# Kernel optimization log

Measured on AMD Instinct MI355X. Metric: run time of the kernel, lower is better.

Reference implementation:

```python
import jax, jax.numpy as jnp
import numpy as np

B, N, D_IN, D_OUT, H = 64, 512, 256, 256, 4
HD = D_OUT // H


def setup_inputs() -> dict:
    key = jax.random.key(0)
    ks = jax.random.split(key, 10)
    x = jax.random.normal(ks[0], (B, N, D_IN), dtype=jnp.float32)
    adj = jax.random.randint(ks[1], (N, N), 0, 2, dtype=jnp.int32)
    adj = adj.at[jnp.arange(N), jnp.arange(N)].set(1)  # self-loops: no empty rows
    s_in = 1.0 / np.sqrt(D_IN)
    s_out = 1.0 / np.sqrt(D_OUT)
    wq = jax.random.uniform(ks[2], (D_OUT, D_IN), jnp.float32, -s_in, s_in)
    bq = jax.random.uniform(ks[3], (D_OUT,), jnp.float32, -s_in, s_in)
    wk = jax.random.uniform(ks[4], (D_OUT, D_IN), jnp.float32, -s_in, s_in)
    bk = jax.random.uniform(ks[5], (D_OUT,), jnp.float32, -s_in, s_in)
    wv = jax.random.uniform(ks[6], (D_OUT, D_IN), jnp.float32, -s_in, s_in)
    bv = jax.random.uniform(ks[7], (D_OUT,), jnp.float32, -s_in, s_in)
    wo = jax.random.uniform(ks[8], (D_OUT, D_OUT), jnp.float32, -s_out, s_out)
    bo = jax.random.uniform(ks[9], (D_OUT,), jnp.float32, -s_out, s_out)
    return {"x": x, "adj": adj, "wq": wq, "bq": bq, "wk": wk, "bk": bk,
            "wv": wv, "bv": bv, "wo": wo, "bo": bo}


def reference(x, adj, wq, bq, wk, bk, wv, bv, wo, bo):
    b, n, _ = x.shape
    # [B,N,D_out] -> [B,H,N,HD]
    q = (x @ wq.T + bq).reshape(b, n, H, HD).transpose(0, 2, 1, 3)
    k = (x @ wk.T + bk).reshape(b, n, H, HD).transpose(0, 2, 1, 3)
    v = (x @ wv.T + bv).reshape(b, n, H, HD).transpose(0, 2, 1, 3)
    scores = jnp.einsum('bhnd,bhmd->bhnm', q, k) / jnp.sqrt(jnp.float32(HD))
    scores = jnp.where(adj[None, None] == 0, -jnp.inf, scores)
    attn = jnp.nan_to_num(jax.nn.softmax(scores, axis=-1), nan=0.0)
    out = jnp.einsum('bhnm,bhmd->bhnd', attn, v)
    out = out.transpose(0, 2, 1, 3).reshape(b, n, D_OUT)
    return out @ wo.T + bo
```

## Files before the change

kernel.cpp:

```cpp
#include <hip/hip_runtime.h>
#include <stdint.h>

typedef float f32x4 __attribute__((ext_vector_type(4)));
typedef short s16x8 __attribute__((ext_vector_type(8)));
typedef unsigned short u16x4 __attribute__((ext_vector_type(4)));
typedef unsigned int u32x4 __attribute__((ext_vector_type(4)));

#define BB 64
#define NN 512
#define DIN 256
#define DOUT 256
#define HH 4
#define HD 64

__device__ __forceinline__ unsigned short f2b(float f) {
  union { float f; unsigned u; } v; v.f = f;
  unsigned r = v.u + 0x7fffu + ((v.u >> 16) & 1u);
  return (unsigned short)(r >> 16);
}
__device__ __forceinline__ void mfma16(f32x4& acc, s16x8 a, s16x8 b) {
  acc = __builtin_amdgcn_mfma_f32_16x16x32_bf16(a, b, acc, 0, 0, 0);
}
__device__ __forceinline__ unsigned cvtpk(float lo, float hi) {
  unsigned r;
  asm("v_cvt_pk_bf16_f32 %0, %1, %2" : "=v"(r) : "v"(lo), "v"(hi));
  return r;
}

__global__ void k_wconv(const float* __restrict__ s0, const float* __restrict__ s1,
                        const float* __restrict__ s2, const float* __restrict__ s3,
                        unsigned short* __restrict__ d0, unsigned short* __restrict__ d1,
                        unsigned short* __restrict__ d2, unsigned short* __restrict__ d3) {
  int b = blockIdx.x;
  int mat = b >> 6;
  int i = (b & 63) * 256 + threadIdx.x;
  const float* s = mat == 0 ? s0 : mat == 1 ? s1 : mat == 2 ? s2 : s3;
  unsigned short* d = mat == 0 ? d0 : mat == 1 ? d1 : mat == 2 ? d2 : d3;
  f32x4 v = ((const f32x4*)s)[i];
  u16x4 o;
  o[0] = f2b(v[0]); o[1] = f2b(v[1]); o[2] = f2b(v[2]); o[3] = f2b(v[3]);
  ((u16x4*)d)[i] = o;
}

__global__ void k_adjbits(const int* __restrict__ adj, unsigned long long* __restrict__ ab) {
  int row = blockIdx.x;
  int w = threadIdx.x >> 6, lane = threadIdx.x & 63;
  int v = adj[row * NN + w * 64 + lane];
  unsigned long long m = __ballot(v != 0);
  if (lane == 0) ab[row * 8 + w] = m;
}

__global__ __launch_bounds__(256, 2) void k_qkv(
    const float* __restrict__ x,
    const unsigned short* __restrict__ wqh,
    const unsigned short* __restrict__ wkh,
    const unsigned short* __restrict__ wvh,
    const float* __restrict__ bq, const float* __restrict__ bk, const float* __restrict__ bv,
    unsigned short* __restrict__ Qb, unsigned short* __restrict__ Kb, unsigned short* __restrict__ Vtb)
{
  __shared__ __align__(16) unsigned char xs[32768];
  __shared__ __align__(16) unsigned char wsl[32768];
  int tid = threadIdx.x, wave = tid >> 6, lane = tid & 63;
  int lr = lane & 15, lk = lane >> 4;
  int t0 = blockIdx.x * 64;

  const float* xsrc = x + (size_t)t0 * DIN;
#pragma unroll
  for (int i = 0; i < 8; ++i) {
    int lin = i * 256 + tid;
    int r = lin >> 5, cc = lin & 31;
    int dst = r * 512 + ((cc ^ (r & 7)) << 4);
    f32x4 a = *(const f32x4*)(xsrc + lin * 8);
    f32x4 b = *(const f32x4*)(xsrc + lin * 8 + 4);
    u32x4 pk;
    pk[0] = cvtpk(a[0], a[1]); pk[1] = cvtpk(a[2], a[3]);
    pk[2] = cvtpk(b[0], b[1]); pk[3] = cvtpk(b[2], b[3]);
    *(u32x4*)(xs + dst) = pk;
    *(s16x8*)(wsl + dst) = *(const s16x8*)(wqh + lin * 8);
  }
  __syncthreads();

  for (int c = 0; c < 12; ++c) {
    int seg = c >> 2, h = c & 3, nb0 = h * 64;
    const float* bias = seg == 0 ? bq : (seg == 1 ? bk : bv);

    s16x8 gw[8];
    if (c < 11) {
      int cn = c + 1, segn = cn >> 2;
      const unsigned short* wn = (segn == 0 ? wqh : segn == 1 ? wkh : wvh) + (size_t)(cn & 3) * 64 * DIN;
#pragma unroll
      for (int i = 0; i < 8; ++i) gw[i] = *(const s16x8*)(wn + (i * 256 + tid) * 8);
    }

    f32x4 acc[4] = {};
    if (seg < 2) {
      int chrow = wave * 16 + lr;
#pragma unroll
      for (int k0 = 0; k0 < 8; ++k0) {
        int cg = k0 * 4 + lk;
        s16x8 a = *(const s16x8*)(wsl + chrow * 512 + ((cg ^ (chrow & 7)) << 4));
#pragma unroll
        for (int ct = 0; ct < 4; ++ct) {
          int tr = ct * 16 + lr;
          s16x8 b = *(const s16x8*)(xs + tr * 512 + ((cg ^ (tr & 7)) << 4));
          mfma16(acc[ct], a, b);
        }
      }
      unsigned short* dst = (seg == 0) ? Qb : Kb;
      f32x4 bv4 = *(const f32x4*)(bias + nb0 + wave * 16 + lk * 4);
#pragma unroll
      for (int ct = 0; ct < 4; ++ct) {
        int n_ = t0 + ct * 16 + lr;
        int b_ = n_ >> 9, nn = n_ & 511;
        u16x4 pk;
#pragma unroll
        for (int j = 0; j < 4; ++j) pk[j] = f2b(acc[ct][j] + bv4[j]);
        *(u16x4*)(dst + ((size_t)(b_ * HH + h) * NN + nn) * HD + wave * 16 + lk * 4) = pk;
      }
    } else {
      int tokrow = wave * 16 + lr;
#pragma unroll
      for (int k0 = 0; k0 < 8; ++k0) {
        int cg = k0 * 4 + lk;
        s16x8 a = *(const s16x8*)(xs + tokrow * 512 + ((cg ^ (tokrow & 7)) << 4));
#pragma unroll
        for (int nt = 0; nt < 4; ++nt) {
          int cr = nt * 16 + lr;
          s16x8 b = *(const s16x8*)(wsl + cr * 512 + ((cg ^ (cr & 7)) << 4));
          mfma16(acc[nt], a, b);
        }
      }
      int m0 = t0 + wave * 16 + lk * 4;
      int b_ = m0 >> 9, n0 = m0 & 511;
#pragma unroll
      for (int nt = 0; nt < 4; ++nt) {
        int hd = nt * 16 + lr;
        float bs = bias[nb0 + hd];
        u16x4 pk;
#pragma unroll
        for (int j = 0; j < 4; ++j) pk[j] = f2b(acc[nt][j] + bs);
        *(u16x4*)(Vtb + ((size_t)(b_ * HH + h) * HD + hd) * NN + n0) = pk;
      }
    }
    __syncthreads();
    if (c < 11) {
#pragma unroll
      for (int i = 0; i < 8; ++i) {
        int lin = i * 256 + tid;
        int r = lin >> 5, cc = lin & 31;
        *(s16x8*)(wsl + r * 512 + ((cc ^ (r & 7)) << 4)) = gw[i];
      }
    }
    __syncthreads();
  }
}

__global__ __launch_bounds__(512, 2) void k_attn(
    const unsigned short* __restrict__ Qb, const unsigned short* __restrict__ Kb,
    const unsigned short* __restrict__ Vtb, const unsigned long long* __restrict__ ab,
    unsigned short* __restrict__ att)
{
  __shared__ __align__(16) unsigned char kl[2][8192];
  __shared__ __align__(16) unsigned char vtl[2][8192];
  __shared__ __align__(16) unsigned char plb[32768];

  int tid = threadIdx.x, wave = tid >> 6, lane = tid & 63;
  int lr = lane & 15, lk = lane >> 4;
  int bid = blockIdx.x;
  int g = bid >> 4, r = bid & 15;
  int bh = g * 8 + (r & 7);
  int qt = r >> 3;
  int h = bh & 3, b_ = bh >> 2;
  const unsigned short* Qp = Qb + (size_t)bh * NN * HD;
  const unsigned short* Kp = Kb + (size_t)bh * NN * HD;
  const unsigned short* Vp = Vtb + (size_t)bh * HD * NN;
  int q0 = qt * 256 + wave * 32;

  s16x8 qa[2][2];
#pragma unroll
  for (int s = 0; s < 2; ++s) {
    qa[s][0] = *(const s16x8*)(Qp + (q0 + s * 16 + lr) * HD + lk * 8);
    qa[s][1] = *(const s16x8*)(Qp + (q0 + s * 16 + lr) * HD + 32 + lk * 8);
  }

  f32x4 oacc[2][4] = {};
  float rs[2] = {0.f, 0.f};
  unsigned char* plw = plb + wave * 4096;
  int sw = (lr & 7) << 4;

  int srow = tid >> 3, scol = tid & 7;
  int sdst = srow * 128 + ((scol * 16) ^ ((srow & 7) << 4));
  const unsigned short* ksrc = Kp + srow * HD + scol * 8;
  const unsigned short* vsrc = Vp + srow * NN + scol * 8;

  *(s16x8*)(kl[0] + sdst)  = *(const s16x8*)ksrc;
  *(s16x8*)(vtl[0] + sdst) = *(const s16x8*)vsrc;
  __syncthreads();

#pragma unroll
  for (int kt = 0; kt < 8; ++kt) {
    unsigned char* klc = kl[kt & 1];
    unsigned char* vtc = vtl[kt & 1];
    unsigned long long abr[2];
#pragma unroll
    for (int s = 0; s < 2; ++s) abr[s] = ab[(size_t)(q0 + s * 16 + lr) * 8 + kt];

#pragma unroll
    for (int s = 0; s < 2; ++s) {
#pragma unroll
      for (int ks = 0; ks < 4; ++ks) {
        int key = ks * 16 + lr;
        s16x8 kb0 = *(const s16x8*)(klc + key * 128 + ((lk * 16) ^ ((key & 7) << 4)));
        s16x8 kb1 = *(const s16x8*)(klc + key * 128 + ((64 + lk * 16) ^ ((key & 7) << 4)));
        f32x4 sx = {};
        mfma16(sx, kb0, qa[s][0]);
        mfma16(sx, kb1, qa[s][1]);
        float p[4];
#pragma unroll
        for (int j = 0; j < 4; ++j)
          p[j] = ((abr[s] >> (ks * 16 + lk * 4 + j)) & 1ULL) ? __expf(sx[j] * 0.125f) : 0.0f;
        unsigned w0 = cvtpk(p[0], p[1]);
        unsigned w1 = cvtpk(p[2], p[3]);
        union { unsigned u; float f; } t0, t1, t2, t3;
        t0.u = w0 << 16; t1.u = w0 & 0xffff0000u;
        t2.u = w1 << 16; t3.u = w1 & 0xffff0000u;
        rs[s] += (t0.f + t1.f) + (t2.f + t3.f);
        uint2 pw; pw.x = w0; pw.y = w1;
        *(uint2*)(plw + s * 2048 + lr * 128 + ((ks * 32 + lk * 8) ^ sw)) = pw;
      }
    }

    s16x8 gk, gv;
    if (kt < 7) {
      gk = *(const s16x8*)(ksrc + (kt + 1) * 64 * HD);
      gv = *(const s16x8*)(vsrc + (kt + 1) * 64);
    }

#pragma unroll
    for (int s = 0; s < 2; ++s) {
      s16x8 pa0 = *(const s16x8*)(plw + s * 2048 + lr * 128 + ((lk * 16) ^ sw));
      s16x8 pa1 = *(const s16x8*)(plw + s * 2048 + lr * 128 + ((64 + lk * 16) ^ sw));
#pragma unroll
      for (int dt = 0; dt < 4; ++dt) {
        int d = dt * 16 + lr;
        s16x8 vb0 = *(const s16x8*)(vtc + d * 128 + ((lk * 16) ^ ((d & 7) << 4)));
        s16x8 vb1 = *(const s16x8*)(vtc + d * 128 + ((64 + lk * 16) ^ ((d & 7) << 4)));
        mfma16(oacc[s][dt], vb0, pa0);
        mfma16(oacc[s][dt], vb1, pa1);
      }
    }
    if (kt < 7) {
      *(s16x8*)(kl[(kt & 1) ^ 1] + sdst)  = gk;
      *(s16x8*)(vtl[(kt & 1) ^ 1] + sdst) = gv;
      __syncthreads();
    }
  }

#pragma unroll
  for (int s = 0; s < 2; ++s) {
    float v = rs[s];
    v += __shfl_xor(v, 16);
    v += __shfl_xor(v, 32);
    float rinv = 1.0f / v;
    int n_ = q0 + s * 16 + lr;
#pragma unroll
    for (int dt = 0; dt < 4; ++dt) {
      uint2 ow;
      ow.x = cvtpk(oacc[s][dt][0] * rinv, oacc[s][dt][1] * rinv);
      ow.y = cvtpk(oacc[s][dt][2] * rinv, oacc[s][dt][3] * rinv);
      *(uint2*)(att + ((size_t)(b_ * NN + n_) * DOUT) + h * HD + dt * 16 + lk * 4) = ow;
    }
  }
}

__global__ __launch_bounds__(256, 2) void k_out(
    const unsigned short* __restrict__ att, const unsigned short* __restrict__ woh,
    const float* __restrict__ bo, float* __restrict__ out)
{
  __shared__ __align__(16) unsigned char as_[32768];
  __shared__ __align__(16) unsigned char wsl[32768];
  int tid = threadIdx.x, wave = tid >> 6, lane = tid & 63;
  int lr = lane & 15, lk = lane >> 4;
  int t0 = blockIdx.x * 64;

  const unsigned short* asrc = att + (size_t)t0 * DOUT;
#pragma unroll
  for (int i = 0; i < 8; ++i) {
    int lin = i * 256 + tid;
    int r = lin >> 5, cc = lin & 31;
    int dst = r * 512 + ((cc ^ (r & 7)) << 4);
    *(s16x8*)(as_ + dst) = *(const s16x8*)(asrc + lin * 8);
    *(s16x8*)(wsl + dst) = *(const s16x8*)(woh + lin * 8);
  }
  __syncthreads();

  for (int c = 0; c < 4; ++c) {
    int nb0 = c * 64;
    s16x8 gw[8];
    if (c < 3) {
      const unsigned short* wn = woh + (size_t)(c + 1) * 64 * DOUT;
#pragma unroll
      for (int i = 0; i < 8; ++i) gw[i] = *(const s16x8*)(wn + (i * 256 + tid) * 8);
    }

    f32x4 acc[4] = {};
    int chrow = wave * 16 + lr;
#pragma unroll
    for (int k0 = 0; k0 < 8; ++k0) {
      int cg = k0 * 4 + lk;
      s16x8 a = *(const s16x8*)(wsl + chrow * 512 + ((cg ^ (chrow & 7)) << 4));
#pragma unroll
      for (int ct = 0; ct < 4; ++ct) {
        int tr = ct * 16 + lr;
        s16x8 b = *(const s16x8*)(as_ + tr * 512 + ((cg ^ (tr & 7)) << 4));
        mfma16(acc[ct], a, b);
      }
    }
    f32x4 bv4 = *(const f32x4*)(bo + nb0 + wave * 16 + lk * 4);
#pragma unroll
    for (int ct = 0; ct < 4; ++ct) {
      int m = t0 + ct * 16 + lr;
      f32x4 o = acc[ct] + bv4;
      *(f32x4*)(out + (size_t)m * DOUT + nb0 + wave * 16 + lk * 4) = o;
    }
    __syncthreads();
    if (c < 3) {
#pragma unroll
      for (int i = 0; i < 8; ++i) {
        int lin = i * 256 + tid;
        int r = lin >> 5, cc = lin & 31;
        *(s16x8*)(wsl + r * 512 + ((cc ^ (r & 7)) << 4)) = gw[i];
      }
    }
    __syncthreads();
  }
}

extern "C" void kernel_launch(void* const* d_in, const int* in_sizes, int n_in,
                              void* d_out, int out_size, void* d_ws, size_t ws_size,
                              hipStream_t stream) {
  const float* x  = (const float*)d_in[0];
  const int*   adj = (const int*)d_in[1];
  const float* wq = (const float*)d_in[2];
  const float* bq = (const float*)d_in[3];
  const float* wk = (const float*)d_in[4];
  const float* bk = (const float*)d_in[5];
  const float* wv = (const float*)d_in[6];
  const float* bv = (const float*)d_in[7];
  const float* wo = (const float*)d_in[8];
  const float* bo = (const float*)d_in[9];
  float* out = (float*)d_out;

  char* ws = (char*)d_ws;
  size_t off = 0;
  auto carve = [&](size_t bytes) -> char* {
    off = (off + 255) & ~(size_t)255;
    char* p = ws + off;
    off += bytes;
    return p;
  };
  unsigned short* wqh  = (unsigned short*)carve((size_t)DOUT * DIN * 2);
  unsigned short* wkh  = (unsigned short*)carve((size_t)DOUT * DIN * 2);
  unsigned short* wvh  = (unsigned short*)carve((size_t)DOUT * DIN * 2);
  unsigned short* woh  = (unsigned short*)carve((size_t)DOUT * DOUT * 2);
  unsigned long long* abits = (unsigned long long*)carve((size_t)NN * 8 * 8);
  unsigned short* Qb   = (unsigned short*)carve((size_t)BB * HH * NN * HD * 2);
  unsigned short* Kb   = (unsigned short*)carve((size_t)BB * HH * NN * HD * 2);
  unsigned short* Vtb  = (unsigned short*)carve((size_t)BB * HH * HD * NN * 2);
  unsigned short* attb = (unsigned short*)carve((size_t)BB * NN * DOUT * 2);

  k_wconv<<<dim3(256), 256, 0, stream>>>(wq, wk, wv, wo, wqh, wkh, wvh, woh);
  k_adjbits<<<dim3(512), 512, 0, stream>>>(adj, abits);
  k_qkv<<<dim3(512), 256, 0, stream>>>(x, wqh, wkh, wvh, bq, bk, bv, Qb, Kb, Vtb);
  k_attn<<<dim3(512), 512, 0, stream>>>(Qb, Kb, Vtb, abits, attb);
  k_out<<<dim3(512), 256, 0, stream>>>(attb, woh, bo, out);
}
```

Baseline: 181.5 us.

## Fold weight bf16 conversion into GEMM kernels and hoist K/V LDS reads

Removes the separate weight-conversion kernel and has k_qkv and k_out load fp32 weights and convert them to bf16 on the fly while staging into LDS. This saves one launch and a workspace round trip, but doubles the global bytes per weight prefetch and doubles the register footprint of the prefetch buffers. Separately, k_attn now loads the K and V^T fragments from LDS once per tile into registers instead of reloading them for each query subtile, cutting LDS reads at the cost of more VGPRs.

Result: no change. 184.5 us (+1.7%).

```diff
diff --git a/kernel.cpp b/kernel.cpp
--- a/kernel.cpp
+++ b/kernel.cpp
@@ -27,21 +27,6 @@
   return r;
 }
 
-__global__ void k_wconv(const float* __restrict__ s0, const float* __restrict__ s1,
-                        const float* __restrict__ s2, const float* __restrict__ s3,
-                        unsigned short* __restrict__ d0, unsigned short* __restrict__ d1,
-                        unsigned short* __restrict__ d2, unsigned short* __restrict__ d3) {
-  int b = blockIdx.x;
-  int mat = b >> 6;
-  int i = (b & 63) * 256 + threadIdx.x;
-  const float* s = mat == 0 ? s0 : mat == 1 ? s1 : mat == 2 ? s2 : s3;
-  unsigned short* d = mat == 0 ? d0 : mat == 1 ? d1 : mat == 2 ? d2 : d3;
-  f32x4 v = ((const f32x4*)s)[i];
-  u16x4 o;
-  o[0] = f2b(v[0]); o[1] = f2b(v[1]); o[2] = f2b(v[2]); o[3] = f2b(v[3]);
-  ((u16x4*)d)[i] = o;
-}
-
 __global__ void k_adjbits(const int* __restrict__ adj, unsigned long long* __restrict__ ab) {
   int row = blockIdx.x;
   int w = threadIdx.x >> 6, lane = threadIdx.x & 63;
@@ -52,9 +37,7 @@
 
 __global__ __launch_bounds__(256, 2) void k_qkv(
     const float* __restrict__ x,
-    const unsigned short* __restrict__ wqh,
-    const unsigned short* __restrict__ wkh,
-    const unsigned short* __restrict__ wvh,
+    const float* __restrict__ wq, const float* __restrict__ wk, const float* __restrict__ wv,
     const float* __restrict__ bq, const float* __restrict__ bk, const float* __restrict__ bv,
     unsigned short* __restrict__ Qb, unsigned short* __restrict__ Kb, unsigned short* __restrict__ Vtb)
 {
@@ -76,7 +59,12 @@
     pk[0] = cvtpk(a[0], a[1]); pk[1] = cvtpk(a[2], a[3]);
     pk[2] = cvtpk(b[0], b[1]); pk[3] = cvtpk(b[2], b[3]);
     *(u32x4*)(xs + dst) = pk;
-    *(s16x8*)(wsl + dst) = *(const s16x8*)(wqh + lin * 8);
+    f32x4 wa = *(const f32x4*)(wq + lin * 8);
+    f32x4 wb = *(const f32x4*)(wq + lin * 8 + 4);
+    u32x4 wp;
+    wp[0] = cvtpk(wa[0], wa[1]); wp[1] = cvtpk(wa[2], wa[3]);
+    wp[2] = cvtpk(wb[0], wb[1]); wp[3] = cvtpk(wb[2], wb[3]);
+    *(u32x4*)(wsl + dst) = wp;
   }
   __syncthreads();
 
@@ -84,12 +72,15 @@
     int seg = c >> 2, h = c & 3, nb0 = h * 64;
     const float* bias = seg == 0 ? bq : (seg == 1 ? bk : bv);
 
-    s16x8 gw[8];
+    f32x4 gwa[8], gwb[8];
     if (c < 11) {
       int cn = c + 1, segn = cn >> 2;
-      const unsigned short* wn = (segn == 0 ? wqh : segn == 1 ? wkh : wvh) + (size_t)(cn & 3) * 64 * DIN;
-#pragma unroll
-      for (int i = 0; i < 8; ++i) gw[i] = *(const s16x8*)(wn + (i * 256 + tid) * 8);
+      const float* wn = (segn == 0 ? wq : segn == 1 ? wk : wv) + (size_t)(cn & 3) * 64 * DIN;
+#pragma unroll
+      for (int i = 0; i < 8; ++i) {
+        gwa[i] = *(const f32x4*)(wn + (i * 256 + tid) * 8);
+        gwb[i] = *(const f32x4*)(wn + (i * 256 + tid) * 8 + 4);
+      }
     }
 
     f32x4 acc[4] = {};
@@ -148,7 +139,10 @@
       for (int i = 0; i < 8; ++i) {
         int lin = i * 256 + tid;
         int r = lin >> 5, cc = lin & 31;
-        *(s16x8*)(wsl + r * 512 + ((cc ^ (r & 7)) << 4)) = gw[i];
+        u32x4 wp;
+        wp[0] = cvtpk(gwa[i][0], gwa[i][1]); wp[1] = cvtpk(gwa[i][2], gwa[i][3]);
+        wp[2] = cvtpk(gwb[i][0], gwb[i][1]); wp[3] = cvtpk(gwb[i][2], gwb[i][3]);
+        *(u32x4*)(wsl + r * 512 + ((cc ^ (r & 7)) << 4)) = wp;
       }
     }
     __syncthreads();
@@ -205,16 +199,21 @@
 #pragma unroll
     for (int s = 0; s < 2; ++s) abr[s] = ab[(size_t)(q0 + s * 16 + lr) * 8 + kt];
 
+    s16x8 kb[4][2];
+#pragma unroll
+    for (int ks = 0; ks < 4; ++ks) {
+      int key = ks * 16 + lr;
+      kb[ks][0] = *(const s16x8*)(klc + key * 128 + ((lk * 16) ^ ((key & 7) << 4)));
+      kb[ks][1] = *(const s16x8*)(klc + key * 128 + ((64 + lk * 16) ^ ((key & 7) << 4)));
+    }
+
 #pragma unroll
     for (int s = 0; s < 2; ++s) {
 #pragma unroll
       for (int ks = 0; ks < 4; ++ks) {
-        int key = ks * 16 + lr;
-        s16x8 kb0 = *(const s16x8*)(klc + key * 128 + ((lk * 16) ^ ((key & 7) << 4)));
-        s16x8 kb1 = *(const s16x8*)(klc + key * 128 + ((64 + lk * 16) ^ ((key & 7) << 4)));
         f32x4 sx = {};
-        mfma16(sx, kb0, qa[s][0]);
-        mfma16(sx, kb1, qa[s][1]);
+        mfma16(sx, kb[ks][0], qa[s][0]);
+        mfma16(sx, kb[ks][1], qa[s][1]);
         float p[4];
 #pragma unroll
         for (int j = 0; j < 4; ++j)
@@ -236,17 +235,21 @@
       gv = *(const s16x8*)(vsrc + (kt + 1) * 64);
     }
 
+    s16x8 vb[4][2];
+#pragma unroll
+    for (int dt = 0; dt < 4; ++dt) {
+      int d = dt * 16 + lr;
+      vb[dt][0] = *(const s16x8*)(vtc + d * 128 + ((lk * 16) ^ ((d & 7) << 4)));
+      vb[dt][1] = *(const s16x8*)(vtc + d * 128 + ((64 + lk * 16) ^ ((d & 7) << 4)));
+    }
 #pragma unroll
     for (int s = 0; s < 2; ++s) {
       s16x8 pa0 = *(const s16x8*)(plw + s * 2048 + lr * 128 + ((lk * 16) ^ sw));
       s16x8 pa1 = *(const s16x8*)(plw + s * 2048 + lr * 128 + ((64 + lk * 16) ^ sw));
 #pragma unroll
       for (int dt = 0; dt < 4; ++dt) {
-        int d = dt * 16 + lr;
-        s16x8 vb0 = *(const s16x8*)(vtc + d * 128 + ((lk * 16) ^ ((d & 7) << 4)));
-        s16x8 vb1 = *(const s16x8*)(vtc + d * 128 + ((64 + lk * 16) ^ ((d & 7) << 4)));
-        mfma16(oacc[s][dt], vb0, pa0);
-        mfma16(oacc[s][dt], vb1, pa1);
+        mfma16(oacc[s][dt], vb[dt][0], pa0);
+        mfma16(oacc[s][dt], vb[dt][1], pa1);
       }
     }
     if (kt < 7) {
@@ -274,7 +277,7 @@
 }
 
 __global__ __launch_bounds__(256, 2) void k_out(
-    const unsigned short* __restrict__ att, const unsigned short* __restrict__ woh,
+    const unsigned short* __restrict__ att, const float* __restrict__ wo,
     const float* __restrict__ bo, float* __restrict__ out)
 {
   __shared__ __align__(16) unsigned char as_[32768];
@@ -290,17 +293,25 @@
     int r = lin >> 5, cc = lin & 31;
     int dst = r * 512 + ((cc ^ (r & 7)) << 4);
     *(s16x8*)(as_ + dst) = *(const s16x8*)(asrc + lin * 8);
-    *(s16x8*)(wsl + dst) = *(const s16x8*)(woh + lin * 8);
+    f32x4 wa = *(const f32x4*)(wo + lin * 8);
+    f32x4 wb = *(const f32x4*)(wo + lin * 8 + 4);
+    u32x4 wp;
+    wp[0] = cvtpk(wa[0], wa[1]); wp[1] = cvtpk(wa[2], wa[3]);
+    wp[2] = cvtpk(wb[0], wb[1]); wp[3] = cvtpk(wb[2], wb[3]);
+    *(u32x4*)(wsl + dst) = wp;
   }
   __syncthreads();
 
   for (int c = 0; c < 4; ++c) {
     int nb0 = c * 64;
-    s16x8 gw[8];
+    f32x4 gwa[8], gwb[8];
     if (c < 3) {
-      const unsigned short* wn = woh + (size_t)(c + 1) * 64 * DOUT;
-#pragma unroll
-      for (int i = 0; i < 8; ++i) gw[i] = *(const s16x8*)(wn + (i * 256 + tid) * 8);
+      const float* wn = wo + (size_t)(c + 1) * 64 * DOUT;
+#pragma unroll
+      for (int i = 0; i < 8; ++i) {
+        gwa[i] = *(const f32x4*)(wn + (i * 256 + tid) * 8);
+        gwb[i] = *(const f32x4*)(wn + (i * 256 + tid) * 8 + 4);
+      }
     }
 
     f32x4 acc[4] = {};
@@ -329,7 +340,10 @@
       for (int i = 0; i < 8; ++i) {
         int lin = i * 256 + tid;
         int r = lin >> 5, cc = lin & 31;
-        *(s16x8*)(wsl + r * 512 + ((cc ^ (r & 7)) << 4)) = gw[i];
+        u32x4 wp;
+        wp[0] = cvtpk(gwa[i][0], gwa[i][1]); wp[1] = cvtpk(gwa[i][2], gwa[i][3]);
+        wp[2] = cvtpk(gwb[i][0], gwb[i][1]); wp[3] = cvtpk(gwb[i][2], gwb[i][3]);
+        *(u32x4*)(wsl + r * 512 + ((cc ^ (r & 7)) << 4)) = wp;
       }
     }
     __syncthreads();
@@ -359,19 +373,14 @@
     off += bytes;
     return p;
   };
-  unsigned short* wqh  = (unsigned short*)carve((size_t)DOUT * DIN * 2);
-  unsigned short* wkh  = (unsigned short*)carve((size_t)DOUT * DIN * 2);
-  unsigned short* wvh  = (unsigned short*)carve((size_t)DOUT * DIN * 2);
-  unsigned short* woh  = (unsigned short*)carve((size_t)DOUT * DOUT * 2);
   unsigned long long* abits = (unsigned long long*)carve((size_t)NN * 8 * 8);
   unsigned short* Qb   = (unsigned short*)carve((size_t)BB * HH * NN * HD * 2);
   unsigned short* Kb   = (unsigned short*)carve((size_t)BB * HH * NN * HD * 2);
   unsigned short* Vtb  = (unsigned short*)carve((size_t)BB * HH * HD * NN * 2);
   unsigned short* attb = (unsigned short*)carve((size_t)BB * NN * DOUT * 2);
 
-  k_wconv<<<dim3(256), 256, 0, stream>>>(wq, wk, wv, wo, wqh, wkh, wvh, woh);
   k_adjbits<<<dim3(512), 512, 0, stream>>>(adj, abits);
-  k_qkv<<<dim3(512), 256, 0, stream>>>(x, wqh, wkh, wvh, bq, bk, bv, Qb, Kb, Vtb);
+  k_qkv<<<dim3(512), 256, 0, stream>>>(x, wq, wk, wv, bq, bk, bv, Qb, Kb, Vtb);
   k_attn<<<dim3(512), 512, 0, stream>>>(Qb, Kb, Vtb, abits, attb);
-  k_out<<<dim3(512), 256, 0, stream>>>(attb, woh, bo, out);
-}
+  k_out<<<dim3(512), 256, 0, stream>>>(attb, wo, bo, out);
+}
```
